# Optimization experiments

Hardware: AMD Instinct MI355X
Metric: run time of the kernel (lower is better)

## Reference

```python
import jax, jax.numpy as jnp
import numpy as np

MS = (1, 2, 4, 8, 16, 32)  # ms_token_size; last entry == H == W
A = -0.75  # PyTorch bicubic coefficient


def _cubic_w(t, a=A):
    t = abs(float(t))
    if t <= 1.0:
        return (a + 2.0) * t**3 - (a + 3.0) * t**2 + 1.0
    if t < 2.0:
        return a * t**3 - 5.0 * a * t**2 + 8.0 * a * t - 4.0 * a
    return 0.0


def _bicubic_matrix(n_in, n_out):
    # Dense [n_out, n_in] matrix reproducing F.interpolate(mode='bicubic',
    # align_corners=False) with border-clamped taps (PyTorch semantics).
    M = np.zeros((n_out, n_in), np.float32)
    s = n_in / n_out
    for i in range(n_out):
        x = (i + 0.5) * s - 0.5
        x0 = int(np.floor(x))
        t = x - x0
        for off in (-1, 0, 1, 2):
            j = min(max(x0 + off, 0), n_in - 1)
            M[i, j] += _cubic_w(off - t)
    return jnp.asarray(M)


def _area_down(x, pn):
    # 'area' interpolation with integer factor == average pooling
    B, C, H, W = x.shape
    f = H // pn
    return x.reshape(B, C, pn, f, pn, f).mean(axis=(3, 5))


def _bicubic_up(x, Mh, Mw):
    # separable bicubic: y = Mh @ x @ Mw^T per (b, c)
    return jnp.einsum('hi,wj,bcij->bchw', Mh, Mw, x)


def setup_inputs() -> dict:
    key = jax.random.key(0)
    k1, k2 = jax.random.split(key)
    z_enc = jax.random.normal(k1, (16, 128, 32, 32), dtype=jnp.float32)
    emb = jax.random.normal(k2, (8192, 128), dtype=jnp.float32) * 1.0  # std=1.0
    return {"z_enc": z_enc, "emb": emb}


def reference(z_enc, emb):
    B, C, H, W = z_enc.shape
    n_levels = len(MS)
    # z_enc is detached in the original (z_enc.detach())
    z_rest = jax.lax.stop_gradient(z_enc)
    z_dec = jnp.zeros_like(z_rest)
    e_sq = jnp.sum(emb * emb, axis=1)  # [V]
    ret = []
    for step, pn in enumerate(MS):
        last = step == n_levels - 1
        zd = z_rest if last else _area_down(z_rest, pn)
        flat = zd.transpose(0, 2, 3, 1).reshape(-1, C)  # [B*pn*pn, C]
        # ||z||^2 + ||e||^2 - 2 z e^T
        dist = jnp.sum(flat * flat, axis=1, keepdims=True) + e_sq \
               - 2.0 * (flat @ emb.T)
        token = jnp.argmin(dist, axis=1)  # [B*pn*pn]
        zq = emb[token].reshape(B, pn, pn, C).transpose(0, 3, 1, 2)  # [B,C,pn,pn]
        if last:
            zu = zq
        else:
            Mh = _bicubic_matrix(pn, H)
            Mw = _bicubic_matrix(pn, W)
            zu = _bicubic_up(zq, Mh, Mw)
        z_dec = z_dec + zu
        z_rest = z_rest - zu
        ret.append(z_dec)
    return jnp.stack(ret)  # [n_levels, B, C, H, W]
```

## Files before the change

kernel.cpp:

```cpp
#include <hip/hip_runtime.h>
#include <hip/hip_bf16.h>

#define NCODES 8192
#define CDIM 128
#define NTOT (16*128*32*32)
#define KTOT 22272

typedef __attribute__((ext_vector_type(8))) short bf16x8;
typedef __attribute__((ext_vector_type(16))) float f32x16;
typedef unsigned long long u64;
typedef unsigned int u32;
typedef unsigned short ushort_t;

__device__ __forceinline__ ushort_t f2bf(float x) {
    u32 u = __float_as_uint(x);
    u32 r = (u + 0x7FFFu + ((u >> 16) & 1u)) >> 16;
    return (ushort_t)r;
}
__device__ __forceinline__ float bf2f(ushort_t h) {
    return __uint_as_float(((u32)h) << 16);
}

__device__ __forceinline__ void gload_lds16(const void* g, void* l) {
    __builtin_amdgcn_global_load_lds(
        (const __attribute__((address_space(1))) unsigned int*)g,
        (__attribute__((address_space(3))) unsigned int*)l, 16, 0, 0);
}

__global__ __launch_bounds__(256) void pack_emb_kernel(const float* __restrict__ src,
        ushort_t* __restrict__ dst, float* __restrict__ esq) {
    __shared__ float sm[32][129];
    int rb = blockIdx.x, t = threadIdx.x;
    int rl = t >> 3, d0 = (t & 7) * 16;
    const float4* s4 = (const float4*)(src + (size_t)(rb * 32 + rl) * CDIM + d0);
    #pragma unroll
    for (int j = 0; j < 4; j++) {
        float4 v = s4[j];
        sm[rl][d0 + 4*j + 0] = v.x; sm[rl][d0 + 4*j + 1] = v.y;
        sm[rl][d0 + 4*j + 2] = v.z; sm[rl][d0 + 4*j + 3] = v.w;
    }
    __syncthreads();
    {
        int r = t >> 3, g = t & 7;
        float s = 0.f;
        #pragma unroll
        for (int k = 0; k < 16; k++) { float x = sm[r][g * 16 + k]; s += x * x; }
        s += __shfl_xor(s, 1, 64);
        s += __shfl_xor(s, 2, 64);
        s += __shfl_xor(s, 4, 64);
        if (g == 0) esq[rb * 32 + r] = s;
    }
    #pragma unroll
    for (int k = 0; k < 2; k++) {
        int s = t + 256 * k;
        int c = s >> 6, l = s & 63;
        int r = l & 31, dbase = c * 16 + (l >> 5) * 8;
        bf16x8 vh, vl;
        #pragma unroll
        for (int e = 0; e < 8; e++) {
            float x = sm[r][dbase + e];
            ushort_t hh = f2bf(x);
            vh[e] = (short)hh;
            vl[e] = (short)f2bf(x - bf2f(hh));
        }
        size_t base = ((size_t)(rb * 8 + c) * 2) * 512 + (size_t)l * 8;
        *(bf16x8*)(dst + base)       = vh;
        *(bf16x8*)(dst + base + 512) = vl;
    }
}

__global__ __launch_bounds__(256) void pack_kernel(const float* __restrict__ src,
        ushort_t* __restrict__ dst) {
    __shared__ float sm[32][129];
    int rb = blockIdx.x, t = threadIdx.x;
    int rl = t >> 3, d0 = (t & 7) * 16;
    const float4* s4 = (const float4*)(src + (size_t)(rb * 32 + rl) * CDIM + d0);
    #pragma unroll
    for (int j = 0; j < 4; j++) {
        float4 v = s4[j];
        sm[rl][d0 + 4*j + 0] = v.x; sm[rl][d0 + 4*j + 1] = v.y;
        sm[rl][d0 + 4*j + 2] = v.z; sm[rl][d0 + 4*j + 3] = v.w;
    }
    __syncthreads();
    #pragma unroll
    for (int k = 0; k < 2; k++) {
        int s = t + 256 * k;
        int c = s >> 6, l = s & 63;
        int r = l & 31, dbase = c * 16 + (l >> 5) * 8;
        bf16x8 vh, vl;
        #pragma unroll
        for (int e = 0; e < 8; e++) {
            float x = sm[r][dbase + e] * -2.0f;
            ushort_t hh = f2bf(x);
            vh[e] = (short)hh;
            vl[e] = (short)f2bf(x - bf2f(hh));
        }
        size_t base = ((size_t)(rb * 8 + c) * 2) * 512 + (size_t)l * 8;
        *(bf16x8*)(dst + base)       = vh;
        *(bf16x8*)(dst + base + 512) = vl;
    }
}

__global__ __launch_bounds__(256) void pack_l5_kernel(const float* __restrict__ src,
        ushort_t* __restrict__ dst) {
    __shared__ float sm[128][36];
    int bh = blockIdx.x;
    int b = bh >> 5, h = bh & 31;
    int t = threadIdx.x;
    int d = t >> 1, w0 = (t & 1) * 16;
    const float* sp = src + (((size_t)b * CDIM + d) * 32 + h) * 32 + w0;
    #pragma unroll
    for (int j = 0; j < 16; j++) sm[d][w0 + j] = sp[j];
    __syncthreads();
    #pragma unroll
    for (int k = 0; k < 2; k++) {
        int s = t + 256 * k;
        int c = s >> 6, l = s & 63;
        int w = l & 31, dbase = c * 16 + (l >> 5) * 8;
        bf16x8 vh, vl;
        #pragma unroll
        for (int e = 0; e < 8; e++) {
            float x = sm[dbase + e][w] * -2.0f;
            ushort_t hh = f2bf(x);
            vh[e] = (short)hh;
            vl[e] = (short)f2bf(x - bf2f(hh));
        }
        size_t base = ((size_t)(bh * 8 + c) * 2) * 512 + (size_t)l * 8;
        *(bf16x8*)(dst + base)       = vh;
        *(bf16x8*)(dst + base + 512) = vl;
    }
}

__global__ __launch_bounds__(256) void down_kernel(const float* __restrict__ src,
        float* __restrict__ zd, u64* __restrict__ keys) {
    int gi = blockIdx.x * 256 + threadIdx.x;
    if (gi < KTOT) keys[gi] = ~0ull;
    int t    = gi;
    int item = t >> 6;
    int wi   = t & 63;
    int row = item >> 7, dim = item & 127;
    const float* sp = src + (((size_t)row * CDIM + dim) * 32) * 32;
    float s = 0.f;
    #pragma unroll
    for (int k = 0; k < 16; k++) {
        int flat = wi * 16 + k;
        s += sp[(flat >> 5) * 32 + (flat & 31)];
    }
    #pragma unroll
    for (int d = 32; d; d >>= 1) s += __shfl_xor(s, d, 64);
    if (wi == 0) zd[(size_t)row * CDIM + dim] = s * (1.0f / 1024.0f);
}

__global__ __launch_bounds__(512) void argmin_kernel(
        const float* __restrict__ zsrc, const ushort_t* __restrict__ bpk,
        const float* __restrict__ esq, u64* __restrict__ keys,
        int tiles, int slices, int nrows) {
    __shared__ ushort_t lds[2][16384];
    __shared__ float es_lds[2048];

    int cps = NCODES / slices;
    int steps = cps >> 6;
    int bid = blockIdx.x;
    int tile  = bid / slices;
    int slice = bid % slices;
    int code0 = slice * cps;
    int tid = threadIdx.x, wv = tid >> 6, l = tid & 63, l31 = l & 31, lh = l >> 5;

    int rb = tile * 8 + wv;
    bf16x8 a_h[8], a_l[8];
    {
        int row = rb * 32 + l31;
        if (row > nrows - 1) row = nrows - 1;
        const float* zr = zsrc + (size_t)row * CDIM + lh * 8;
        #pragma unroll
        for (int c = 0; c < 8; c++) {
            float4 f0 = *(const float4*)(zr + c * 16);
            float4 f1 = *(const float4*)(zr + c * 16 + 4);
            float xs[8] = {f0.x, f0.y, f0.z, f0.w, f1.x, f1.y, f1.z, f1.w};
            #pragma unroll
            for (int e = 0; e < 8; e++) {
                float x = -2.0f * xs[e];
                ushort_t hh = f2bf(x);
                a_h[c][e] = (short)hh;
                a_l[c][e] = (short)f2bf(x - bf2f(hh));
            }
        }
    }
    float ev0 = 0.f, ev1 = 0.f, ev2 = 0.f, ev3 = 0.f;
    if (tid < cps)        ev0 = esq[code0 + tid];
    if (512  + tid < cps) ev1 = esq[code0 + 512 + tid];
    if (1024 + tid < cps) ev2 = esq[code0 + 1024 + tid];
    if (1536 + tid < cps) ev3 = esq[code0 + 1536 + tid];
    __builtin_amdgcn_sched_barrier(0);

    const char* bbase = (const char*)bpk + (size_t)(code0 >> 6) * 32768;
    {
        const char* g0 = bbase + (size_t)wv * 4096 + (size_t)l * 16;
        ushort_t* d0 = &lds[0][wv * 2048];
        gload_lds16(g0,        d0);
        gload_lds16(g0 + 1024, d0 + 512);
        gload_lds16(g0 + 2048, d0 + 1024);
        gload_lds16(g0 + 3072, d0 + 1536);
    }
    __builtin_amdgcn_sched_barrier(0);
    if (tid < cps)        es_lds[tid] = ev0;
    if (512  + tid < cps) es_lds[512 + tid] = ev1;
    if (1024 + tid < cps) es_lds[1024 + tid] = ev2;
    if (1536 + tid < cps) es_lds[1536 + tid] = ev3;
    asm volatile("s_waitcnt lgkmcnt(0)" ::: "memory");

    float best[16];
    int   bidx[16];
    #pragma unroll
    for (int r = 0; r < 16; r++) { best[r] = 1e38f; bidx[r] = 0; }

    for (int t = 0; t < steps; ++t) {
        asm volatile("s_waitcnt vmcnt(0)" ::: "memory");
        __builtin_amdgcn_s_barrier();
        if (t + 1 < steps) {
            const char* g = bbase + (size_t)(t + 1) * 32768
                          + (size_t)wv * 4096 + (size_t)l * 16;
            ushort_t* d = &lds[(t + 1) & 1][wv * 2048];
            gload_lds16(g,        d);
            gload_lds16(g + 1024, d + 512);
            gload_lds16(g + 2048, d + 1024);
            gload_lds16(g + 3072, d + 1536);
        }
        float es0 = es_lds[(t << 6) + l31];
        float es1 = es_lds[(t << 6) + 32 + l31];
        f32x16 acc0, acc1;
        #pragma unroll
        for (int r = 0; r < 16; r++) { acc0[r] = es0; acc1[r] = es1; }
        const ushort_t* lp = &lds[t & 1][0] + l * 8;
        __builtin_amdgcn_s_setprio(1);
        #pragma unroll
        for (int c = 0; c < 8; c++) {
            bf16x8 g0h = *(const bf16x8*)(lp + (2 * c) * 512);
            bf16x8 g0l = *(const bf16x8*)(lp + (2 * c + 1) * 512);
            bf16x8 g1h = *(const bf16x8*)(lp + 8192 + (2 * c) * 512);
            bf16x8 g1l = *(const bf16x8*)(lp + 8192 + (2 * c + 1) * 512);
            acc0 = __builtin_amdgcn_mfma_f32_32x32x16_bf16(a_h[c], g0h, acc0, 0, 0, 0);
            acc1 = __builtin_amdgcn_mfma_f32_32x32x16_bf16(a_h[c], g1h, acc1, 0, 0, 0);
            acc0 = __builtin_amdgcn_mfma_f32_32x32x16_bf16(a_h[c], g0l, acc0, 0, 0, 0);
            acc1 = __builtin_amdgcn_mfma_f32_32x32x16_bf16(a_h[c], g1l, acc1, 0, 0, 0);
            acc0 = __builtin_amdgcn_mfma_f32_32x32x16_bf16(a_l[c], g0h, acc0, 0, 0, 0);
            acc1 = __builtin_amdgcn_mfma_f32_32x32x16_bf16(a_l[c], g1h, acc1, 0, 0, 0);
        }
        __builtin_amdgcn_s_setprio(0);
        int code = code0 + (t << 6) + l31;
        #pragma unroll
        for (int r = 0; r < 16; r++) {
            float s0 = acc0[r], s1 = acc1[r];
            float m  = fminf(s0, s1);
            int   ci = (s0 <= s1) ? code : code + 32;
            bool lt = m < best[r];
            best[r] = lt ? m : best[r];
            bidx[r] = lt ? ci : bidx[r];
        }
    }

    #pragma unroll
    for (int r = 0; r < 16; r++) {
        u32 fb = __float_as_uint(best[r]);
        fb = (fb & 0x80000000u) ? ~fb : (fb | 0x80000000u);
        u64 key = ((u64)fb << 32) | (u32)bidx[r];
        #pragma unroll
        for (int d = 1; d < 32; d <<= 1) {
            u64 o = __shfl_xor(key, d, 64);
            key = (o < key) ? o : key;
        }
        if (l31 == 0) {
            int rw = tile * 256 + wv * 32 + (r & 3) + 8 * (r >> 2) + 4 * lh;
            atomicMin(&keys[rw], key);
        }
    }
}

__global__ __launch_bounds__(512) void argmin64_kernel(
        const ushort_t* __restrict__ apk, const ushort_t* __restrict__ bpk,
        const float* __restrict__ esq, u64* __restrict__ keys,
        int tiles, int slices) {
    __shared__ ushort_t lds[2][16384];
    __shared__ float es_lds[1024];

    int cps = NCODES / slices;
    int steps = cps >> 6;
    int bid = blockIdx.x;
    int tile  = bid / slices;
    int slice = bid % slices;
    int code0 = slice * cps;
    int tid = threadIdx.x, wv = tid >> 6, l = tid & 63, l31 = l & 31, lh = l >> 5;

    int rb0 = tile * 16 + wv * 2;
    const ushort_t* ap = apk + (size_t)rb0 * 8192 + l * 8;
    bf16x8 a0h[8], a0l[8], a1h[8], a1l[8];
    #pragma unroll
    for (int c = 0; c < 8; c++) {
        a0h[c] = *(const bf16x8*)(ap + (2 * c) * 512);
        a0l[c] = *(const bf16x8*)(ap + (2 * c + 1) * 512);
        a1h[c] = *(const bf16x8*)(ap + 8192 + (2 * c) * 512);
        a1l[c] = *(const bf16x8*)(ap + 8192 + (2 * c + 1) * 512);
    }
    float ev0 = 0.f, ev1 = 0.f;
    if (tid < cps)       ev0 = esq[code0 + tid];
    if (512 + tid < cps) ev1 = esq[code0 + 512 + tid];
    __builtin_amdgcn_sched_barrier(0);

    const char* bbase = (const char*)bpk + (size_t)(code0 >> 6) * 32768;
    {
        const char* g0 = bbase + (size_t)wv * 4096 + (size_t)l * 16;
        ushort_t* d0 = &lds[0][wv * 2048];
        gload_lds16(g0,        d0);
        gload_lds16(g0 + 1024, d0 + 512);
        gload_lds16(g0 + 2048, d0 + 1024);
        gload_lds16(g0 + 3072, d0 + 1536);
    }
    __builtin_amdgcn_sched_barrier(0);
    if (tid < cps)       es_lds[tid] = ev0;
    if (512 + tid < cps) es_lds[512 + tid] = ev1;
    asm volatile("s_waitcnt lgkmcnt(0)" ::: "memory");

    float best[32];
    int   bidx[32];
    #pragma unroll
    for (int r = 0; r < 32; r++) { best[r] = 1e38f; bidx[r] = 0; }

    for (int t = 0; t < steps; ++t) {
        asm volatile("s_waitcnt vmcnt(0)" ::: "memory");
        __builtin_amdgcn_s_barrier();
        if (t + 1 < steps) {
            const char* g = bbase + (size_t)(t + 1) * 32768
                          + (size_t)wv * 4096 + (size_t)l * 16;
            ushort_t* d = &lds[(t + 1) & 1][wv * 2048];
            gload_lds16(g,        d);
            gload_lds16(g + 1024, d + 512);
            gload_lds16(g + 2048, d + 1024);
            gload_lds16(g + 3072, d + 1536);
        }
        const ushort_t* lpb = &lds[t & 1][0] + l * 8;
        __builtin_amdgcn_s_setprio(1);
        #pragma unroll
        for (int g = 0; g < 2; g++) {
            float es = es_lds[(t << 6) + (g << 5) + l31];
            f32x16 acc0, acc1;
            #pragma unroll
            for (int r = 0; r < 16; r++) { acc0[r] = es; acc1[r] = es; }
            const ushort_t* lp = lpb + g * 8192;
            #pragma unroll
            for (int c = 0; c < 8; c++) {
                bf16x8 gh = *(const bf16x8*)(lp + (2 * c) * 512);
                bf16x8 gl = *(const bf16x8*)(lp + (2 * c + 1) * 512);
                acc0 = __builtin_amdgcn_mfma_f32_32x32x16_bf16(a0h[c], gh, acc0, 0, 0, 0);
                acc1 = __builtin_amdgcn_mfma_f32_32x32x16_bf16(a1h[c], gh, acc1, 0, 0, 0);
                acc0 = __builtin_amdgcn_mfma_f32_32x32x16_bf16(a0h[c], gl, acc0, 0, 0, 0);
                acc1 = __builtin_amdgcn_mfma_f32_32x32x16_bf16(a1h[c], gl, acc1, 0, 0, 0);
                acc0 = __builtin_amdgcn_mfma_f32_32x32x16_bf16(a0l[c], gh, acc0, 0, 0, 0);
                acc1 = __builtin_amdgcn_mfma_f32_32x32x16_bf16(a1l[c], gh, acc1, 0, 0, 0);
            }
            int code = code0 + (t << 6) + (g << 5) + l31;
            #pragma unroll
            for (int r = 0; r < 16; r++) {
                float s0 = acc0[r];
                bool lt0 = s0 < best[r];
                best[r] = lt0 ? s0 : best[r];
                bidx[r] = lt0 ? code : bidx[r];
                float s1 = acc1[r];
                bool lt1 = s1 < best[16 + r];
                best[16 + r] = lt1 ? s1 : best[16 + r];
                bidx[16 + r] = lt1 ? code : bidx[16 + r];
            }
        }
        __builtin_amdgcn_s_setprio(0);
    }

    #pragma unroll
    for (int rt = 0; rt < 2; rt++) {
        #pragma unroll
        for (int r = 0; r < 16; r++) {
            u32 fb = __float_as_uint(best[rt * 16 + r]);
            fb = (fb & 0x80000000u) ? ~fb : (fb | 0x80000000u);
            u64 key = ((u64)fb << 32) | (u32)bidx[rt * 16 + r];
            #pragma unroll
            for (int d = 1; d < 32; d <<= 1) {
                u64 o = __shfl_xor(key, d, 64);
                key = (o < key) ? o : key;
            }
            if (l31 == 0) {
                int rw = tile * 512 + wv * 64 + rt * 32
                       + (r & 3) + 8 * (r >> 2) + 4 * lh;
                atomicMin(&keys[rw], key);
            }
        }
    }
}

__device__ __forceinline__ float cubicw(float t) {
    float t2 = t * t;
    if (t <= 1.0f) return (1.25f * t - 2.25f) * t2 + 1.0f;
    return -0.75f * (((t - 5.0f) * t + 8.0f) * t - 4.0f);
}

__global__ __launch_bounds__(256) void up_kernel(
        const float* __restrict__ emb,
        const u64* __restrict__ keys,
        const float* __restrict__ src,
        const float* __restrict__ prev,
        float* __restrict__ zrest,
        float* __restrict__ out,
        float* __restrict__ zd_next,
        int pn, int last, int first, int pnn) {
    __shared__ float wtab[32][4];
    __shared__ int   itab[32][4];
    __shared__ float smp[512];
    int tid = threadIdx.x;
    if (!last && tid < 128) {
        int pos = tid >> 2, tap = tid & 3;
        float s  = (float)pn * (1.0f / 32.0f);
        float x  = ((float)pos + 0.5f) * s - 0.5f;
        float x0 = floorf(x);
        float t  = x - x0;
        int   off = tap - 1;
        float w  = cubicw(fabsf((float)off - t));
        int   jj = (int)x0 + off;
        jj = min(max(jj, 0), pn - 1);
        wtab[pos][tap] = w;
        itab[pos][tap] = jj;
    }
    __syncthreads();

    int t  = blockIdx.x * 256 + tid;
    int w4 = (t & 7) << 2;
    int h  = (t >> 3) & 31;
    int c  = (t >> 8) & 127;
    int b  = t >> 15;
    size_t i = (((size_t)b * CDIM + c) * 32 + h) * 32 + w4;

    float zu[4];
    if (last) {
        int kb = (b << 10) + (h << 5) + w4;
        #pragma unroll
        for (int j = 0; j < 4; j++) {
            int tok = (int)(keys[kb + j] & 0xFFFFFFFFull);
            zu[j] = emb[(size_t)tok * CDIM + c];
        }
    } else {
        int base = b * pn * pn;
        #pragma unroll
        for (int j = 0; j < 4; j++) zu[j] = 0.f;
        #pragma unroll
        for (int u = 0; u < 4; u++) {
            float whu = wtab[h][u];
            int   ih  = itab[h][u] * pn;
            #pragma unroll
            for (int j = 0; j < 4; j++) {
                float acc = 0.f;
                #pragma unroll
                for (int v = 0; v < 4; v++) {
                    int tok = (int)(keys[base + ih + itab[w4 + j][v]] & 0xFFFFFFFFull);
                    acc += wtab[w4 + j][v] * emb[(size_t)tok * CDIM + c];
                }
                zu[j] += whu * acc;
            }
        }
    }
    float4 sv = *(const float4*)(src + i);
    float4 pv = {0.f, 0.f, 0.f, 0.f};
    if (!first) pv = *(const float4*)(prev + i);
    float4 ov, rv;
    ov.x = pv.x + zu[0]; ov.y = pv.y + zu[1]; ov.z = pv.z + zu[2]; ov.w = pv.w + zu[3];
    rv.x = sv.x - zu[0]; rv.y = sv.y - zu[1]; rv.z = sv.z - zu[2]; rv.w = sv.w - zu[3];
    *(float4*)(out + i)   = ov;
    *(float4*)(zrest + i) = rv;

    if (pnn) {
        int f = 32 / pnn;
        if (f >= 4) {
            smp[h * 8 + (w4 >> 2)] = (rv.x + rv.y) + (rv.z + rv.w);
        } else {
            smp[h * 16 + (w4 >> 1)]     = rv.x + rv.y;
            smp[h * 16 + (w4 >> 1) + 1] = rv.z + rv.w;
        }
        __syncthreads();
        int W = pnn * pnn;
        if (tid < W) {
            int lb = __builtin_ctz(pnn);
            int ph = tid >> lb, pw = tid & (pnn - 1);
            float s = 0.f;
            if (f >= 4) {
                int cg = f >> 2;
                for (int u = 0; u < f; u++)
                    for (int v = 0; v < cg; v++)
                        s += smp[(ph * f + u) * 8 + pw * cg + v];
            } else {
                s = smp[(2 * ph) * 16 + pw] + smp[(2 * ph + 1) * 16 + pw];
            }
            int b2 = blockIdx.x >> 7, c2 = blockIdx.x & 127;
            int row = (b2 * pnn + ph) * pnn + pw;
            zd_next[(size_t)row * CDIM + c2] = s * (1.0f / (float)(f * f));
        }
    }
}

extern "C" void kernel_launch(void* const* d_in, const int* in_sizes, int n_in,
                              void* d_out, int out_size, void* d_ws, size_t ws_size,
                              hipStream_t stream) {
    const float* z_enc = (const float*)d_in[0];
    const float* emb   = (const float*)d_in[1];
    float* out = (float*)d_out;
    float* ws  = (float*)d_ws;

    float*    zrest  = ws;
    float*    zd_f32 = ws + 2097152;
    ushort_t* emb_pk = (ushort_t*)(ws + 4194304);
    ushort_t* zd_pk  = (ushort_t*)(ws + 5242880);
    float*    esq    = ws + 7340032;
    u64*      keys   = (u64*)(ws + 7348224);

    pack_emb_kernel<<<NCODES / 32, 256, 0, stream>>>(emb, emb_pk, esq);
    down_kernel<<<512, 256, 0, stream>>>(z_enc, zd_f32, keys);

    const int MS_[6]   = {1, 2, 4, 8, 16, 32};
    const int SL_[6]   = {128, 128, 128, 64, 32, 8};
    const int KOFF_[6] = {0, 256, 512, 768, 1792, 5888};
    for (int lvl = 0; lvl < 6; lvl++) {
        int pn     = MS_[lvl];
        int rows   = 16 * pn * pn;
        int slices = SL_[lvl];
        const float* src = lvl ? zrest : z_enc;

        if (lvl < 4) {
            int tiles = (rows + 255) / 256;
            argmin_kernel<<<tiles * slices, 512, 0, stream>>>(
                zd_f32, emb_pk, esq, keys + KOFF_[lvl], tiles, slices, rows);
        } else {
            int tiles = rows / 512;
            if (lvl == 4) pack_kernel<<<rows / 32, 256, 0, stream>>>(zd_f32, zd_pk);
            else          pack_l5_kernel<<<512, 256, 0, stream>>>(zrest, zd_pk);
            argmin64_kernel<<<tiles * slices, 512, 0, stream>>>(
                zd_pk, emb_pk, esq, keys + KOFF_[lvl], tiles, slices);
        }
        int pnn = (lvl < 4) ? MS_[lvl + 1] : 0;
        up_kernel<<<NTOT / 4 / 256, 256, 0, stream>>>(
            emb, keys + KOFF_[lvl], src, lvl ? (out + (size_t)(lvl - 1) * NTOT) : out,
            zrest, out + (size_t)lvl * NTOT, zd_f32,
            pn, lvl == 5 ? 1 : 0, lvl == 0 ? 1 : 0, pnn);
    }
}
```

Baseline: 434.4 us.

## Deepen codebook LDS pipeline to six 32-code stages with prefetch distance four

Replaces the double-buffered 64-code LDS staging in the argmin kernel with a six-slot ring of 32-code buffers, prefetching four stages ahead and processing two stages per barrier. The goal is to hide global-to-LDS load latency more fully and halve barrier frequency per code. In exchange it uses more LDS (96KB vs 64KB), which may lower occupancy, and adds modulo buffer bookkeeping.

```diff
diff --git a/kernel.cpp b/kernel.cpp
--- a/kernel.cpp
+++ b/kernel.cpp
@@ -280,11 +280,11 @@
         const ushort_t* __restrict__ apk, const ushort_t* __restrict__ bpk,
         const float* __restrict__ esq, u64* __restrict__ keys,
         int tiles, int slices) {
-    __shared__ ushort_t lds[2][16384];
+    __shared__ ushort_t lds[6][8192];
     __shared__ float es_lds[1024];
 
     int cps = NCODES / slices;
-    int steps = cps >> 6;
+    int steps = cps >> 5;
     int bid = blockIdx.x;
     int tile  = bid / slices;
     int slice = bid % slices;
@@ -306,71 +306,81 @@
     if (512 + tid < cps) ev1 = esq[code0 + 512 + tid];
     __builtin_amdgcn_sched_barrier(0);
 
-    const char* bbase = (const char*)bpk + (size_t)(code0 >> 6) * 32768;
-    {
-        const char* g0 = bbase + (size_t)wv * 4096 + (size_t)l * 16;
-        ushort_t* d0 = &lds[0][wv * 2048];
-        gload_lds16(g0,        d0);
-        gload_lds16(g0 + 1024, d0 + 512);
-        gload_lds16(g0 + 2048, d0 + 1024);
-        gload_lds16(g0 + 3072, d0 + 1536);
+    const char* bbase = (const char*)bpk + (size_t)(code0 >> 5) * 16384;
+    int issue = wv * 2;
+
+    #pragma unroll
+    for (int s = 0; s < 4; s++) {
+        if (s < steps) {
+            const char* g = bbase + (size_t)s * 16384 + (size_t)issue * 1024
+                          + (size_t)l * 16;
+            ushort_t* d = &lds[s][issue * 512];
+            gload_lds16(g, d);
+            gload_lds16(g + 1024, d + 512);
+        }
     }
     __builtin_amdgcn_sched_barrier(0);
     if (tid < cps)       es_lds[tid] = ev0;
     if (512 + tid < cps) es_lds[512 + tid] = ev1;
-    asm volatile("s_waitcnt lgkmcnt(0)" ::: "memory");
+    asm volatile("s_waitcnt vmcnt(0) lgkmcnt(0)" ::: "memory");
+    __builtin_amdgcn_s_barrier();
 
     float best[32];
     int   bidx[32];
     #pragma unroll
     for (int r = 0; r < 32; r++) { best[r] = 1e38f; bidx[r] = 0; }
 
-    for (int t = 0; t < steps; ++t) {
+    auto stage = [&](int s, ushort_t* buf) {
+        const char* g = bbase + (size_t)s * 16384 + (size_t)issue * 1024
+                      + (size_t)l * 16;
+        ushort_t* d = buf + issue * 512;
+        gload_lds16(g, d);
+        gload_lds16(g + 1024, d + 512);
+    };
+    auto do_step = [&](int t, const ushort_t* buf) {
+        float es = es_lds[(t << 5) + l31];
+        f32x16 acc0, acc1;
+        #pragma unroll
+        for (int r = 0; r < 16; r++) { acc0[r] = es; acc1[r] = es; }
+        const ushort_t* lp = buf + l * 8;
+        __builtin_amdgcn_s_setprio(1);
+        #pragma unroll
+        for (int c = 0; c < 8; c++) {
+            bf16x8 gh = *(const bf16x8*)(lp + (2 * c) * 512);
+            bf16x8 gl = *(const bf16x8*)(lp + (2 * c + 1) * 512);
+            acc0 = __builtin_amdgcn_mfma_f32_32x32x16_bf16(a0h[c], gh, acc0, 0, 0, 0);
+            acc1 = __builtin_amdgcn_mfma_f32_32x32x16_bf16(a1h[c], gh, acc1, 0, 0, 0);
+            acc0 = __builtin_amdgcn_mfma_f32_32x32x16_bf16(a0h[c], gl, acc0, 0, 0, 0);
+            acc1 = __builtin_amdgcn_mfma_f32_32x32x16_bf16(a1h[c], gl, acc1, 0, 0, 0);
+            acc0 = __builtin_amdgcn_mfma_f32_32x32x16_bf16(a0l[c], gh, acc0, 0, 0, 0);
+            acc1 = __builtin_amdgcn_mfma_f32_32x32x16_bf16(a1l[c], gh, acc1, 0, 0, 0);
+        }
+        __builtin_amdgcn_s_setprio(0);
+        int code = code0 + (t << 5) + l31;
+        #pragma unroll
+        for (int r = 0; r < 16; r++) {
+            float s0 = acc0[r];
+            bool lt0 = s0 < best[r];
+            best[r] = lt0 ? s0 : best[r];
+            bidx[r] = lt0 ? code : bidx[r];
+            float s1 = acc1[r];
+            bool lt1 = s1 < best[16 + r];
+            best[16 + r] = lt1 ? s1 : best[16 + r];
+            bidx[16 + r] = lt1 ? code : bidx[16 + r];
+        }
+    };
+
+    int b0 = 0;
+    for (int p = 0; p < steps; p += 2) {
+        int s4 = b0 + 4; if (s4 >= 6) s4 -= 6;
+        int s5 = s4 + 1; if (s5 >= 6) s5 -= 6;
+        if (p + 4 < steps) stage(p + 4, &lds[0][0] + s4 * 8192);
+        if (p + 5 < steps) stage(p + 5, &lds[0][0] + s5 * 8192);
+        do_step(p,     &lds[0][0] + b0 * 8192);
+        do_step(p + 1, &lds[0][0] + (b0 + 1) * 8192);
         asm volatile("s_waitcnt vmcnt(0)" ::: "memory");
         __builtin_amdgcn_s_barrier();
-        if (t + 1 < steps) {
-            const char* g = bbase + (size_t)(t + 1) * 32768
-                          + (size_t)wv * 4096 + (size_t)l * 16;
-            ushort_t* d = &lds[(t + 1) & 1][wv * 2048];
-            gload_lds16(g,        d);
-            gload_lds16(g + 1024, d + 512);
-            gload_lds16(g + 2048, d + 1024);
-            gload_lds16(g + 3072, d + 1536);
-        }
-        const ushort_t* lpb = &lds[t & 1][0] + l * 8;
-        __builtin_amdgcn_s_setprio(1);
-        #pragma unroll
-        for (int g = 0; g < 2; g++) {
-            float es = es_lds[(t << 6) + (g << 5) + l31];
-            f32x16 acc0, acc1;
-            #pragma unroll
-            for (int r = 0; r < 16; r++) { acc0[r] = es; acc1[r] = es; }
-            const ushort_t* lp = lpb + g * 8192;
-            #pragma unroll
-            for (int c = 0; c < 8; c++) {
-                bf16x8 gh = *(const bf16x8*)(lp + (2 * c) * 512);
-                bf16x8 gl = *(const bf16x8*)(lp + (2 * c + 1) * 512);
-                acc0 = __builtin_amdgcn_mfma_f32_32x32x16_bf16(a0h[c], gh, acc0, 0, 0, 0);
-                acc1 = __builtin_amdgcn_mfma_f32_32x32x16_bf16(a1h[c], gh, acc1, 0, 0, 0);
-                acc0 = __builtin_amdgcn_mfma_f32_32x32x16_bf16(a0h[c], gl, acc0, 0, 0, 0);
-                acc1 = __builtin_amdgcn_mfma_f32_32x32x16_bf16(a1h[c], gl, acc1, 0, 0, 0);
-                acc0 = __builtin_amdgcn_mfma_f32_32x32x16_bf16(a0l[c], gh, acc0, 0, 0, 0);
-                acc1 = __builtin_amdgcn_mfma_f32_32x32x16_bf16(a1l[c], gh, acc1, 0, 0, 0);
-            }
-            int code = code0 + (t << 6) + (g << 5) + l31;
-            #pragma unroll
-            for (int r = 0; r < 16; r++) {
-                float s0 = acc0[r];
-                bool lt0 = s0 < best[r];
-                best[r] = lt0 ? s0 : best[r];
-                bidx[r] = lt0 ? code : bidx[r];
-                float s1 = acc1[r];
-                bool lt1 = s1 < best[16 + r];
-                best[16 + r] = lt1 ? s1 : best[16 + r];
-                bidx[16 + r] = lt1 ? code : bidx[16 + r];
-            }
-        }
-        __builtin_amdgcn_s_setprio(0);
+        b0 += 2; if (b0 >= 6) b0 = 0;
     }
 
     #pragma unroll
```

New measurement: 488.5 us. 1.12x slower.

## Fuse packing into up_kernel epilogue and merge init kernels

Applied to the files above, without the earlier changes.

Merges the embedding pack and the down-sampling/key-init kernels into one launch, and removes the separate pack kernels for levels 4 and 5. The bf16 hi/lo packing of the next level's query is now written directly from up_kernel's epilogue, either from the pooled means or from the residual. This saves three launches and the extra global round trip through zd_f32/zrest reads. In exchange, the level-5 pack uses scattered 2-byte stores from up_kernel, which are less coalesced.

```diff
diff --git a/kernel.cpp b/kernel.cpp
--- a/kernel.cpp
+++ b/kernel.cpp
@@ -20,135 +20,72 @@
 __device__ __forceinline__ float bf2f(ushort_t h) {
     return __uint_as_float(((u32)h) << 16);
 }
-
 __device__ __forceinline__ void gload_lds16(const void* g, void* l) {
     __builtin_amdgcn_global_load_lds(
         (const __attribute__((address_space(1))) unsigned int*)g,
         (__attribute__((address_space(3))) unsigned int*)l, 16, 0, 0);
 }
 
-__global__ __launch_bounds__(256) void pack_emb_kernel(const float* __restrict__ src,
-        ushort_t* __restrict__ dst, float* __restrict__ esq) {
-    __shared__ float sm[32][129];
-    int rb = blockIdx.x, t = threadIdx.x;
-    int rl = t >> 3, d0 = (t & 7) * 16;
-    const float4* s4 = (const float4*)(src + (size_t)(rb * 32 + rl) * CDIM + d0);
-    #pragma unroll
-    for (int j = 0; j < 4; j++) {
-        float4 v = s4[j];
-        sm[rl][d0 + 4*j + 0] = v.x; sm[rl][d0 + 4*j + 1] = v.y;
-        sm[rl][d0 + 4*j + 2] = v.z; sm[rl][d0 + 4*j + 3] = v.w;
-    }
-    __syncthreads();
-    {
-        int r = t >> 3, g = t & 7;
+__global__ __launch_bounds__(256) void init_kernel(const float* __restrict__ emb,
+        const float* __restrict__ z_enc, ushort_t* __restrict__ emb_pk,
+        float* __restrict__ esq, float* __restrict__ zd, u64* __restrict__ keys) {
+    int bid = blockIdx.x, t = threadIdx.x;
+    if (bid < 256) {
+        __shared__ float sm[32][129];
+        int rb = bid;
+        int rl = t >> 3, d0 = (t & 7) * 16;
+        const float4* s4 = (const float4*)(emb + (size_t)(rb * 32 + rl) * CDIM + d0);
+        #pragma unroll
+        for (int j = 0; j < 4; j++) {
+            float4 v = s4[j];
+            sm[rl][d0 + 4*j + 0] = v.x; sm[rl][d0 + 4*j + 1] = v.y;
+            sm[rl][d0 + 4*j + 2] = v.z; sm[rl][d0 + 4*j + 3] = v.w;
+        }
+        __syncthreads();
+        {
+            int r = t >> 3, g = t & 7;
+            float s = 0.f;
+            #pragma unroll
+            for (int k = 0; k < 16; k++) { float x = sm[r][g * 16 + k]; s += x * x; }
+            s += __shfl_xor(s, 1, 64);
+            s += __shfl_xor(s, 2, 64);
+            s += __shfl_xor(s, 4, 64);
+            if (g == 0) esq[rb * 32 + r] = s;
+        }
+        #pragma unroll
+        for (int k = 0; k < 2; k++) {
+            int s = t + 256 * k;
+            int c = s >> 6, l = s & 63;
+            int r = l & 31, dbase = c * 16 + (l >> 5) * 8;
+            bf16x8 vh, vl;
+            #pragma unroll
+            for (int e = 0; e < 8; e++) {
+                float x = sm[r][dbase + e];
+                ushort_t hh = f2bf(x);
+                vh[e] = (short)hh;
+                vl[e] = (short)f2bf(x - bf2f(hh));
+            }
+            size_t base = ((size_t)(rb * 8 + c) * 2) * 512 + (size_t)l * 8;
+            *(bf16x8*)(emb_pk + base)       = vh;
+            *(bf16x8*)(emb_pk + base + 512) = vl;
+        }
+    } else {
+        int gi = (bid - 256) * 256 + t;
+        if (gi < KTOT) keys[gi] = ~0ull;
+        int item = gi >> 6;
+        int wi   = gi & 63;
+        int row = item >> 7, dim = item & 127;
+        const float* sp = z_enc + (((size_t)row * CDIM + dim) * 32) * 32;
         float s = 0.f;
         #pragma unroll
-        for (int k = 0; k < 16; k++) { float x = sm[r][g * 16 + k]; s += x * x; }
-        s += __shfl_xor(s, 1, 64);
-        s += __shfl_xor(s, 2, 64);
-        s += __shfl_xor(s, 4, 64);
-        if (g == 0) esq[rb * 32 + r] = s;
-    }
-    #pragma unroll
-    for (int k = 0; k < 2; k++) {
-        int s = t + 256 * k;
-        int c = s >> 6, l = s & 63;
-        int r = l & 31, dbase = c * 16 + (l >> 5) * 8;
-        bf16x8 vh, vl;
-        #pragma unroll
-        for (int e = 0; e < 8; e++) {
-            float x = sm[r][dbase + e];
-            ushort_t hh = f2bf(x);
-            vh[e] = (short)hh;
-            vl[e] = (short)f2bf(x - bf2f(hh));
-        }
-        size_t base = ((size_t)(rb * 8 + c) * 2) * 512 + (size_t)l * 8;
-        *(bf16x8*)(dst + base)       = vh;
-        *(bf16x8*)(dst + base + 512) = vl;
-    }
-}
-
-__global__ __launch_bounds__(256) void pack_kernel(const float* __restrict__ src,
-        ushort_t* __restrict__ dst) {
-    __shared__ float sm[32][129];
-    int rb = blockIdx.x, t = threadIdx.x;
-    int rl = t >> 3, d0 = (t & 7) * 16;
-    const float4* s4 = (const float4*)(src + (size_t)(rb * 32 + rl) * CDIM + d0);
-    #pragma unroll
-    for (int j = 0; j < 4; j++) {
-        float4 v = s4[j];
-        sm[rl][d0 + 4*j + 0] = v.x; sm[rl][d0 + 4*j + 1] = v.y;
-        sm[rl][d0 + 4*j + 2] = v.z; sm[rl][d0 + 4*j + 3] = v.w;
-    }
-    __syncthreads();
-    #pragma unroll
-    for (int k = 0; k < 2; k++) {
-        int s = t + 256 * k;
-        int c = s >> 6, l = s & 63;
-        int r = l & 31, dbase = c * 16 + (l >> 5) * 8;
-        bf16x8 vh, vl;
-        #pragma unroll
-        for (int e = 0; e < 8; e++) {
-            float x = sm[r][dbase + e] * -2.0f;
-            ushort_t hh = f2bf(x);
-            vh[e] = (short)hh;
-            vl[e] = (short)f2bf(x - bf2f(hh));
-        }
-        size_t base = ((size_t)(rb * 8 + c) * 2) * 512 + (size_t)l * 8;
-        *(bf16x8*)(dst + base)       = vh;
-        *(bf16x8*)(dst + base + 512) = vl;
-    }
-}
-
-__global__ __launch_bounds__(256) void pack_l5_kernel(const float* __restrict__ src,
-        ushort_t* __restrict__ dst) {
-    __shared__ float sm[128][36];
-    int bh = blockIdx.x;
-    int b = bh >> 5, h = bh & 31;
-    int t = threadIdx.x;
-    int d = t >> 1, w0 = (t & 1) * 16;
-    const float* sp = src + (((size_t)b * CDIM + d) * 32 + h) * 32 + w0;
-    #pragma unroll
-    for (int j = 0; j < 16; j++) sm[d][w0 + j] = sp[j];
-    __syncthreads();
-    #pragma unroll
-    for (int k = 0; k < 2; k++) {
-        int s = t + 256 * k;
-        int c = s >> 6, l = s & 63;
-        int w = l & 31, dbase = c * 16 + (l >> 5) * 8;
-        bf16x8 vh, vl;
-        #pragma unroll
-        for (int e = 0; e < 8; e++) {
-            float x = sm[dbase + e][w] * -2.0f;
-            ushort_t hh = f2bf(x);
-            vh[e] = (short)hh;
-            vl[e] = (short)f2bf(x - bf2f(hh));
-        }
-        size_t base = ((size_t)(bh * 8 + c) * 2) * 512 + (size_t)l * 8;
-        *(bf16x8*)(dst + base)       = vh;
-        *(bf16x8*)(dst + base + 512) = vl;
-    }
-}
-
-__global__ __launch_bounds__(256) void down_kernel(const float* __restrict__ src,
-        float* __restrict__ zd, u64* __restrict__ keys) {
-    int gi = blockIdx.x * 256 + threadIdx.x;
-    if (gi < KTOT) keys[gi] = ~0ull;
-    int t    = gi;
-    int item = t >> 6;
-    int wi   = t & 63;
-    int row = item >> 7, dim = item & 127;
-    const float* sp = src + (((size_t)row * CDIM + dim) * 32) * 32;
-    float s = 0.f;
-    #pragma unroll
-    for (int k = 0; k < 16; k++) {
-        int flat = wi * 16 + k;
-        s += sp[(flat >> 5) * 32 + (flat & 31)];
-    }
-    #pragma unroll
-    for (int d = 32; d; d >>= 1) s += __shfl_xor(s, d, 64);
-    if (wi == 0) zd[(size_t)row * CDIM + dim] = s * (1.0f / 1024.0f);
+        for (int k = 0; k < 16; k++) {
+            int flat = wi * 16 + k;
+            s += sp[(flat >> 5) * 32 + (flat & 31)];
+        }
+        #pragma unroll
+        for (int d = 32; d; d >>= 1) s += __shfl_xor(s, d, 64);
+        if (wi == 0) zd[(size_t)row * CDIM + dim] = s * (1.0f / 1024.0f);
+    }
 }
 
 __global__ __launch_bounds__(512) void argmin_kernel(
@@ -408,7 +345,8 @@
         float* __restrict__ zrest,
         float* __restrict__ out,
         float* __restrict__ zd_next,
-        int pn, int last, int first, int pnn) {
+        ushort_t* __restrict__ pk,
+        int pn, int last, int first, int pnn, int pkmode) {
     __shared__ float wtab[32][4];
     __shared__ int   itab[32][4];
     __shared__ float smp[512];
@@ -472,6 +410,22 @@
     *(float4*)(out + i)   = ov;
     *(float4*)(zrest + i) = rv;
 
+    if (pkmode == 2) {
+        int rb = b * 32 + h;
+        int cfrag = c >> 4, sub = (c >> 3) & 1, e = c & 7;
+        size_t fbase = ((size_t)(rb * 8 + cfrag) * 2) * 512 + (size_t)e;
+        float rvs[4] = {rv.x, rv.y, rv.z, rv.w};
+        #pragma unroll
+        for (int j = 0; j < 4; j++) {
+            float x = rvs[j] * -2.0f;
+            ushort_t hh = f2bf(x);
+            ushort_t ll = f2bf(x - bf2f(hh));
+            size_t o = fbase + (size_t)(sub * 32 + w4 + j) * 8;
+            pk[o]       = hh;
+            pk[o + 512] = ll;
+        }
+    }
+
     if (pnn) {
         int f = 32 / pnn;
         if (f >= 4) {
@@ -496,7 +450,20 @@
             }
             int b2 = blockIdx.x >> 7, c2 = blockIdx.x & 127;
             int row = (b2 * pnn + ph) * pnn + pw;
-            zd_next[(size_t)row * CDIM + c2] = s * (1.0f / (float)(f * f));
+            float m = s * (1.0f / (float)(f * f));
+            if (pkmode == 1) {
+                float x = m * -2.0f;
+                ushort_t hh = f2bf(x);
+                ushort_t ll = f2bf(x - bf2f(hh));
+                int rb = row >> 5, rr = row & 31;
+                int cfrag = c2 >> 4, sub = (c2 >> 3) & 1, e = c2 & 7;
+                size_t o = ((size_t)(rb * 8 + cfrag) * 2) * 512
+                         + (size_t)(sub * 32 + rr) * 8 + e;
+                pk[o]       = hh;
+                pk[o + 512] = ll;
+            } else {
+                zd_next[(size_t)row * CDIM + c2] = m;
+            }
         }
     }
 }
@@ -516,8 +483,7 @@
     float*    esq    = ws + 7340032;
     u64*      keys   = (u64*)(ws + 7348224);
 
-    pack_emb_kernel<<<NCODES / 32, 256, 0, stream>>>(emb, emb_pk, esq);
-    down_kernel<<<512, 256, 0, stream>>>(z_enc, zd_f32, keys);
+    init_kernel<<<768, 256, 0, stream>>>(emb, z_enc, emb_pk, esq, zd_f32, keys);
 
     const int MS_[6]   = {1, 2, 4, 8, 16, 32};
     const int SL_[6]   = {128, 128, 128, 64, 32, 8};
@@ -534,15 +500,14 @@
                 zd_f32, emb_pk, esq, keys + KOFF_[lvl], tiles, slices, rows);
         } else {
             int tiles = rows / 512;
-            if (lvl == 4) pack_kernel<<<rows / 32, 256, 0, stream>>>(zd_f32, zd_pk);
-            else          pack_l5_kernel<<<512, 256, 0, stream>>>(zrest, zd_pk);
             argmin64_kernel<<<tiles * slices, 512, 0, stream>>>(
                 zd_pk, emb_pk, esq, keys + KOFF_[lvl], tiles, slices);
         }
         int pnn = (lvl < 4) ? MS_[lvl + 1] : 0;
+        int pkmode = (lvl == 3) ? 1 : ((lvl == 4) ? 2 : 0);
         up_kernel<<<NTOT / 4 / 256, 256, 0, stream>>>(
             emb, keys + KOFF_[lvl], src, lvl ? (out + (size_t)(lvl - 1) * NTOT) : out,
-            zrest, out + (size_t)lvl * NTOT, zd_f32,
-            pn, lvl == 5 ? 1 : 0, lvl == 0 ? 1 : 0, pnn);
-    }
-}
+            zrest, out + (size_t)lvl * NTOT, zd_f32, zd_pk,
+            pn, lvl == 5 ? 1 : 0, lvl == 0 ? 1 : 0, pnn, pkmode);
+    }
+}
```

After: 436.1 us. Within noise of the previous version (+0.4%).
